# Kernel optimization log

Measured on AMD Instinct MI355X. Metric: run time of the kernel, lower is better.

The kernel has to match this reference:

```python
import jax, jax.numpy as jnp
import numpy as np

N, E, F_IN, D, D_OUT = 100000, 1600000, 64, 20, 16
EPS = 1e-5


def _mean_agg(x, src, dst, n):
    # gather source features, scatter-mean onto destination nodes
    s = jax.ops.segment_sum(x[src], dst, num_segments=n)
    cnt = jax.ops.segment_sum(jnp.ones((src.shape[0], 1), x.dtype), dst, num_segments=n)
    return s / jnp.maximum(cnt, 1.0)


def _batchnorm(h, g, b):
    mu = jnp.mean(h, axis=0)
    var = jnp.mean(jnp.square(h - mu), axis=0)  # biased variance, BatchNorm1d training math
    return (h - mu) * jax.lax.rsqrt(var + EPS) * g + b


def _block(x, src, dst, Wl, bl, Wr, Ws, bs, Wn, bn, g, be):
    # SAGEConv: lin_l(mean_agg) + lin_r(x); plus linskip; then lin, BN, ReLU
    agg = _mean_agg(x, src, dst, N)
    h = agg @ Wl + bl + x @ Wr + x @ Ws + bs
    h = h @ Wn + bn
    return jax.nn.relu(_batchnorm(h, g, be))


def setup_inputs() -> dict:
    key = jax.random.key(0)
    ks = jax.random.split(key, 32)
    sc = lambda fi: 1.0 / np.sqrt(fi)
    d = {}
    d["x"] = jax.random.normal(ks[0], (N, F_IN), jnp.float32)
    d["edge_index"] = jax.random.randint(ks[1], (2, E), 0, N, dtype=jnp.int64)
    d["edge_attr"] = jax.random.normal(ks[2], (E, 1), jnp.float32)
    # layer 1 (in = F_IN)
    d["Wl1"] = jax.random.normal(ks[3], (F_IN, D), jnp.float32) * sc(F_IN)
    d["bl1"] = jnp.zeros((D,), jnp.float32)
    d["Wr1"] = jax.random.normal(ks[4], (F_IN, D), jnp.float32) * sc(F_IN)
    d["Ws1"] = jax.random.normal(ks[5], (F_IN, D), jnp.float32) * sc(F_IN)
    d["bs1"] = jnp.zeros((D,), jnp.float32)
    d["Wn1"] = jax.random.normal(ks[6], (D, D), jnp.float32) * sc(D)
    d["bn1"] = jnp.zeros((D,), jnp.float32)
    d["g1"] = jnp.ones((D,), jnp.float32)
    d["be1"] = jnp.zeros((D,), jnp.float32)
    # layers 2-4 stacked (in = D)
    d["Wlm"] = jax.random.normal(ks[7], (3, D, D), jnp.float32) * sc(D)
    d["blm"] = jnp.zeros((3, D), jnp.float32)
    d["Wrm"] = jax.random.normal(ks[8], (3, D, D), jnp.float32) * sc(D)
    d["Wsm"] = jax.random.normal(ks[9], (3, D, D), jnp.float32) * sc(D)
    d["bsm"] = jnp.zeros((3, D), jnp.float32)
    d["Wnm"] = jax.random.normal(ks[10], (3, D, D), jnp.float32) * sc(D)
    d["bnm"] = jnp.zeros((3, D), jnp.float32)
    d["gm"] = jnp.ones((3, D), jnp.float32)
    d["bem"] = jnp.zeros((3, D), jnp.float32)
    # layer 5 (no BN/ReLU, out = D_OUT)
    d["Wl5"] = jax.random.normal(ks[11], (D, D), jnp.float32) * sc(D)
    d["bl5"] = jnp.zeros((D,), jnp.float32)
    d["Wr5"] = jax.random.normal(ks[12], (D, D), jnp.float32) * sc(D)
    d["Ws5"] = jax.random.normal(ks[13], (D, D), jnp.float32) * sc(D)
    d["bs5"] = jnp.zeros((D,), jnp.float32)
    d["Wn5"] = jax.random.normal(ks[14], (D, D_OUT), jnp.float32) * sc(D)
    d["bn5"] = jnp.zeros((D_OUT,), jnp.float32)
    return d


def reference(x, edge_index, edge_attr,
              Wl1, bl1, Wr1, Ws1, bs1, Wn1, bn1, g1, be1,
              Wlm, blm, Wrm, Wsm, bsm, Wnm, bnm, gm, bem,
              Wl5, bl5, Wr5, Ws5, bs5, Wn5, bn5):
    src, dst = edge_index[0], edge_index[1]
    # edge_attr is accepted by the torch forward but unused
    h = _block(x, src, dst, Wl1, bl1, Wr1, Ws1, bs1, Wn1, bn1, g1, be1)
    for i in range(3):  # layers 2-4
        h = _block(h, src, dst, Wlm[i], blm[i], Wrm[i], Wsm[i], bsm[i],
                   Wnm[i], bnm[i], gm[i], bem[i])
    # layer 5: sage + skip, final linear, no norm/relu
    agg = _mean_agg(h, src, dst, N)
    h = agg @ Wl5 + bl5 + h @ Wr5 + h @ Ws5 + bs5
    return h @ Wn5 + bn5
```

## Files before the change

### kernel.cpp

```cpp
#include <hip/hip_runtime.h>

constexpr int Nn   = 100000;
constexpr int Ne   = 1600000;
constexpr int FINN = 64;
constexpr int Dh   = 20;
constexpr int Dout = 16;
constexpr float EPSV = 1e-5f;

constexpr int NR  = 16;
constexpr int RSZ = Nn / NR;
constexpr int NSL = 32;
constexpr int P1B = 400;
constexpr int P1E = Ne / P1B;

constexpr size_t OFF_WC1  = 0;
constexpr size_t OFF_C1   = 2560;
constexpr size_t OFF_WCM  = 2592;
constexpr size_t OFF_CM   = 4992;
constexpr size_t OFF_WC5  = 5088;
constexpr size_t OFF_C5   = 5728;
constexpr size_t OFF_ST   = 5760;
constexpr size_t OFF_OFFS = 8192;
constexpr size_t OFF_BSUM = 208896;
constexpr size_t OFF_CNT  = 209408;
constexpr size_t OFF_CSR  = 309760;
constexpr size_t OFF_XA   = 1910784;
constexpr size_t OFF_XB   = 3510784;
constexpr size_t OFF_HP   = 5110784;
constexpr size_t OFF_BHT  = OFF_HP;
constexpr size_t OFF_OBHT = OFF_HP + 6400;
constexpr size_t OFF_RB   = OFF_HP + 12800;

__device__ inline unsigned short f2b(float x) {
    unsigned b = __float_as_uint(x);
    return (unsigned short)((b + 0x7FFFu + ((b >> 16) & 1u)) >> 16);
}
__device__ inline float b2f(unsigned short u) {
    return __uint_as_float(((unsigned)u) << 16);
}
__device__ inline float blo(unsigned u) { return __uint_as_float(u << 16); }
__device__ inline float bhi(unsigned u) { return __uint_as_float(u & 0xFFFF0000u); }
__device__ inline unsigned bpack(float lo, float hi) {
    return (unsigned)f2b(lo) | ((unsigned)f2b(hi) << 16);
}

__global__ void prep_weights(
    const float* __restrict__ Wl1, const float* __restrict__ bl1,
    const float* __restrict__ Wr1, const float* __restrict__ Ws1,
    const float* __restrict__ bs1, const float* __restrict__ Wn1,
    const float* __restrict__ bn1,
    const float* __restrict__ Wlm, const float* __restrict__ blm,
    const float* __restrict__ Wrm, const float* __restrict__ Wsm,
    const float* __restrict__ bsm, const float* __restrict__ Wnm,
    const float* __restrict__ bnm,
    const float* __restrict__ Wl5, const float* __restrict__ bl5,
    const float* __restrict__ Wr5, const float* __restrict__ Ws5,
    const float* __restrict__ bs5, const float* __restrict__ Wn5,
    const float* __restrict__ bn5,
    float* __restrict__ wc1, float* __restrict__ c1,
    float* __restrict__ wcm, float* __restrict__ cm,
    float* __restrict__ wc5, float* __restrict__ c5)
{
    int layer = blockIdx.x;
    int t = threadIdx.x;
    if (layer == 0) {
        for (int idx = t; idx < FINN * Dh; idx += blockDim.x) {
            int k = idx / Dh, j = idx % Dh;
            float a = 0.f, b = 0.f;
            for (int d = 0; d < Dh; ++d) {
                float wn = Wn1[d * Dh + j];
                a += Wl1[k * Dh + d] * wn;
                b += (Wr1[k * Dh + d] + Ws1[k * Dh + d]) * wn;
            }
            wc1[k * 40 + j] = a;
            wc1[k * 40 + 20 + j] = b;
        }
        for (int j = t; j < Dh; j += blockDim.x) {
            float c0 = 0.f;
            for (int d = 0; d < Dh; ++d) c0 += (bl1[d] + bs1[d]) * Wn1[d * Dh + j];
            c1[j] = c0 + bn1[j];
        }
    } else if (layer <= 3) {
        int i = layer - 1;
        const float* Wl = Wlm + i * Dh * Dh;
        const float* Wr = Wrm + i * Dh * Dh;
        const float* Ws = Wsm + i * Dh * Dh;
        const float* Wn = Wnm + i * Dh * Dh;
        const float* bl = blm + i * Dh;
        const float* bs = bsm + i * Dh;
        const float* bn = bnm + i * Dh;
        float* wc = wcm + i * 800;
        float* cc = cm + i * 32;
        for (int idx = t; idx < Dh * Dh; idx += blockDim.x) {
            int k = idx / Dh, j = idx % Dh;
            float a = 0.f, b = 0.f;
            for (int d = 0; d < Dh; ++d) {
                float wn = Wn[d * Dh + j];
                a += Wl[k * Dh + d] * wn;
                b += (Wr[k * Dh + d] + Ws[k * Dh + d]) * wn;
            }
            wc[k * 40 + j] = a;
            wc[k * 40 + 20 + j] = b;
        }
        for (int j = t; j < Dh; j += blockDim.x) {
            float c0 = 0.f;
            for (int d = 0; d < Dh; ++d) c0 += (bl[d] + bs[d]) * Wn[d * Dh + j];
            cc[j] = c0 + bn[j];
        }
    } else {
        for (int idx = t; idx < Dh * Dout; idx += blockDim.x) {
            int k = idx / Dout, j = idx % Dout;
            float a = 0.f, b = 0.f;
            for (int d = 0; d < Dh; ++d) {
                float wn = Wn5[d * Dout + j];
                a += Wl5[k * Dh + d] * wn;
                b += (Wr5[k * Dh + d] + Ws5[k * Dh + d]) * wn;
            }
            wc5[k * 32 + j] = a;
            wc5[k * 32 + 16 + j] = b;
        }
        for (int j = t; j < Dout; j += blockDim.x) {
            float c0 = 0.f;
            for (int d = 0; d < Dh; ++d) c0 += (bl5[d] + bs5[d]) * Wn5[d * Dout + j];
            c5[j] = c0 + bn5[j];
        }
    }
}

__global__ __launch_bounds__(256) void hist1(const int* __restrict__ dst, unsigned* __restrict__ bhT) {
    __shared__ unsigned h[16 * NR];
    int b = blockIdx.x, t = threadIdx.x;
    for (int i = t; i < 16 * NR; i += 256) h[i] = 0;
    __syncthreads();
    int sub = t & 15;
    int e0 = b * P1E, e1 = min(e0 + P1E, Ne);
    for (int e = e0 + t; e < e1; e += 256) {
        int r = dst[e] / RSZ;
        atomicAdd(&h[sub * NR + r], 1u);
    }
    __syncthreads();
    if (t < NR) {
        unsigned s = 0;
        for (int i = 0; i < 16; ++i) s += h[i * NR + t];
        bhT[t * P1B + b] = s;
    }
}

__global__ __launch_bounds__(1024) void scan1(
    const unsigned* __restrict__ bhT, unsigned* __restrict__ obhT, unsigned* __restrict__ rbase)
{
    __shared__ unsigned rtot[NR];
    int t = threadIdx.x;
    int w = t >> 6, lane = t & 63;
    constexpr int PER = (P1B + 63) / 64;
    if (w < NR) {
        unsigned v[PER];
        unsigned s = 0;
#pragma unroll
        for (int i = 0; i < PER; ++i) {
            int b = lane * PER + i;
            v[i] = (b < P1B) ? bhT[w * P1B + b] : 0u;
            s += v[i];
        }
        unsigned val = s;
        for (int off = 1; off < 64; off <<= 1) {
            unsigned u = __shfl_up(val, off, 64);
            if (lane >= off) val += u;
        }
        unsigned run = val - s;
#pragma unroll
        for (int i = 0; i < PER; ++i) {
            int b = lane * PER + i;
            if (b < P1B) obhT[w * P1B + b] = run;
            run += v[i];
        }
        if (lane == 63) rtot[w] = val;
    }
    __syncthreads();
    if (t == 0) {
        unsigned base = 0;
        for (int r = 0; r < NR; ++r) { rbase[r] = base; base += rtot[r]; }
        rbase[NR] = base;
    }
}

__global__ __launch_bounds__(256) void scatter1(
    const int* __restrict__ src, const int* __restrict__ dst,
    const unsigned* __restrict__ obhT, const unsigned* __restrict__ rbase,
    unsigned* __restrict__ ebuf)
{
    __shared__ unsigned cur[NR];
    int b = blockIdx.x, t = threadIdx.x;
    if (t < NR) cur[t] = rbase[t] + obhT[t * P1B + b];
    __syncthreads();
    int e0 = b * P1E, e1 = min(e0 + P1E, Ne);
    for (int e = e0 + t; e < e1; e += 256) {
        int d = dst[e];
        int r = d / RSZ;
        unsigned dl = (unsigned)(d - r * RSZ);
        unsigned pos = atomicAdd(&cur[r], 1u);
        ebuf[pos] = (dl << 17) | (unsigned)src[e];
    }
}

__global__ __launch_bounds__(256) void hist2(
    const unsigned* __restrict__ ebuf, const unsigned* __restrict__ rbase,
    unsigned short* __restrict__ part)
{
    __shared__ unsigned h[RSZ];
    int b = blockIdx.x, t = threadIdx.x;
    int r = b % NR, s = b / NR;
    for (int i = t; i < RSZ; i += 256) h[i] = 0;
    __syncthreads();
    unsigned lo = rbase[r], hi = rbase[r + 1];
    unsigned step = (hi - lo + NSL - 1) / NSL;
    unsigned e0 = lo + (unsigned)s * step;
    unsigned e1 = e0 + step; if (e1 > hi) e1 = hi;
    for (unsigned e = e0 + t; e < e1; e += 256)
        atomicAdd(&h[ebuf[e] >> 17], 1u);
    __syncthreads();
    unsigned short* p = part + (size_t)b * RSZ;
    for (int i = t; i < RSZ; i += 256) p[i] = (unsigned short)h[i];
}

__global__ void col_prefix(unsigned short* __restrict__ part, unsigned* __restrict__ cnt) {
    int d = blockIdx.x * blockDim.x + threadIdx.x;
    if (d >= Nn) return;
    int r = d / RSZ, dl = d - r * RSZ;
    unsigned run = 0;
#pragma unroll
    for (int s = 0; s < NSL; ++s) {
        size_t idx = ((size_t)s * NR + r) * RSZ + dl;
        unsigned v = part[idx];
        part[idx] = (unsigned short)run;
        run += v;
    }
    cnt[d] = run;
}

__global__ void scan_blocksums(const unsigned* __restrict__ cnt, unsigned* __restrict__ bsum, int n) {
    __shared__ unsigned sd[256];
    int b = blockIdx.x, t = threadIdx.x;
    int base = b * 1024;
    unsigned s = 0;
    for (int i = t; i < 1024; i += 256) {
        int idx = base + i;
        if (idx < n) s += cnt[idx];
    }
    sd[t] = s;
    __syncthreads();
    for (int off = 128; off > 0; off >>= 1) {
        if (t < off) sd[t] += sd[t + off];
        __syncthreads();
    }
    if (t == 0) bsum[b] = sd[0];
}

__global__ void scan_bsum(unsigned* __restrict__ bsum, int nb) {
    __shared__ unsigned sh[128];
    int t = threadIdx.x;
    unsigned v = (t < nb) ? bsum[t] : 0u;
    sh[t] = v;
    __syncthreads();
    for (int off = 1; off < 128; off <<= 1) {
        unsigned add = (t >= off) ? sh[t - off] : 0u;
        __syncthreads();
        sh[t] += add;
        __syncthreads();
    }
    if (t < nb) bsum[t] = sh[t] - v;
}

__global__ void scan_final(const unsigned* __restrict__ cnt, const unsigned* __restrict__ bsum,
                           unsigned* __restrict__ offs, int n) {
    __shared__ unsigned wsum[4], woff[4];
    int b = blockIdx.x, t = threadIdx.x;
    int base = b * 1024 + t * 4;
    unsigned v[4];
    unsigned s = 0;
#pragma unroll
    for (int i = 0; i < 4; ++i) {
        int idx = base + i;
        v[i] = (idx < n) ? cnt[idx] : 0u;
        s += v[i];
    }
    unsigned lane = t & 63;
    int w = t >> 6;
    unsigned val = s;
    for (int off = 1; off < 64; off <<= 1) {
        unsigned u = __shfl_up(val, off, 64);
        if (lane >= off) val += u;
    }
    if (lane == 63) wsum[w] = val;
    __syncthreads();
    if (t == 0) {
        unsigned r = 0;
        for (int i = 0; i < 4; ++i) { woff[i] = r; r += wsum[i]; }
    }
    __syncthreads();
    unsigned run = bsum[b] + woff[w] + (val - s);
#pragma unroll
    for (int i = 0; i < 4; ++i) {
        int idx = base + i;
        if (idx < n) {
            offs[idx] = run;
            run += v[i];
            if (idx == n - 1) offs[n] = run;
        }
    }
}

__global__ __launch_bounds__(256) void fill2(
    const unsigned* __restrict__ ebuf, const unsigned* __restrict__ rbase,
    const unsigned* __restrict__ offs, const unsigned short* __restrict__ part,
    unsigned* __restrict__ csr)
{
    __shared__ unsigned cur[RSZ];
    int b = blockIdx.x, t = threadIdx.x;
    int r = b % NR, s = b / NR;
    int lon = r * RSZ;
    const unsigned short* p = part + (size_t)b * RSZ;
    for (int i = t; i < RSZ; i += 256)
        cur[i] = offs[lon + i] + p[i];
    __syncthreads();
    unsigned lo = rbase[r], hi = rbase[r + 1];
    unsigned step = (hi - lo + NSL - 1) / NSL;
    unsigned e0 = lo + (unsigned)s * step;
    unsigned e1 = e0 + step; if (e1 > hi) e1 = hi;
    for (unsigned e = e0 + t; e < e1; e += 256) {
        unsigned v = ebuf[e];
        unsigned pos = atomicAdd(&cur[v >> 17], 1u);
        csr[pos] = v & 0x1FFFFu;
    }
}

template <int FINt, int FO, bool NORM, bool INBF16>
__global__ __launch_bounds__(256) void gemm_kernel(
    const void* __restrict__ xin_, const float* __restrict__ stats,
    const float* __restrict__ g, const float* __restrict__ be,
    const float* __restrict__ wc, const float* __restrict__ cvec,
    unsigned short* __restrict__ xa, unsigned short* __restrict__ xb)
{
    constexpr int XS  = ((FO + 7) / 8) * 8;
    constexpr int XSI = ((FINt + 7) / 8) * 8;
    constexpr int CH  = XS / 8;
    constexpr int CL  = 2 * CH;
    __shared__ float swl[FINt * 2 * FO + 8];
    __shared__ float sscale[Dh], sshift[Dh];
    int t = threadIdx.x;
    for (int i = t; i < FINt * 2 * FO; i += 256) swl[i] = wc[i];
    if (t < 8) swl[FINt * 2 * FO + t] = 0.f;
    if (NORM) {
        if (t < Dh) {
            float mu = stats[t] * (1.0f / Nn);
            float var = stats[32 + t] * (1.0f / Nn) - mu * mu;
            float sc = g[t] * rsqrtf(var + EPSV);
            sscale[t] = sc;
            sshift[t] = be[t] - mu * sc;
        }
    }
    __syncthreads();
    int tid = blockIdx.x * 256 + t;
    int n = tid / CL;
    int c = tid % CL;
    if (n >= Nn) return;
    int half = c / CH, cc = c % CH;
    int off = half * FO + cc * 8;
    int jmax = (cc == CH - 1) ? (FO - (CH - 1) * 8) : 8;

    float acc[8];
#pragma unroll
    for (int j = 0; j < 8; ++j) acc[j] = 0.f;

#pragma unroll
    for (int k4 = 0; k4 < FINt / 4; ++k4) {
        float xs[4];
        if (INBF16) {
            const unsigned short* xr = (const unsigned short*)xin_ + (size_t)n * XSI;
            ushort4 v = *(const ushort4*)(xr + 4 * k4);
            xs[0] = b2f(v.x); xs[1] = b2f(v.y); xs[2] = b2f(v.z); xs[3] = b2f(v.w);
        } else {
            const float* xr = (const float*)xin_ + (size_t)n * FINt;
            float4 v = *(const float4*)(xr + 4 * k4);
            xs[0] = v.x; xs[1] = v.y; xs[2] = v.z; xs[3] = v.w;
        }
        if (NORM) {
#pragma unroll
            for (int kk = 0; kk < 4; ++kk)
                xs[kk] = fmaxf(xs[kk] * sscale[4 * k4 + kk] + sshift[4 * k4 + kk], 0.0f);
        }
#pragma unroll
        for (int kk = 0; kk < 4; ++kk) {
            float xk = xs[kk];
            const float* wr = &swl[(4 * k4 + kk) * (2 * FO) + off];
#pragma unroll
            for (int j = 0; j < 8; ++j) acc[j] = fmaf(xk, wr[j], acc[j]);
        }
    }

    float hv[8];
#pragma unroll
    for (int j = 0; j < 8; ++j) hv[j] = acc[j];
    if (half) {
#pragma unroll
        for (int j = 0; j < 8; ++j) hv[j] += cvec[cc * 8 + j];
    }
#pragma unroll
    for (int j = 0; j < 8; ++j) if (j >= jmax) hv[j] = 0.f;

    unsigned short* dstp = (half ? xb : xa) + (size_t)n * XS + cc * 8;
    uint4 w;
    w.x = bpack(hv[0], hv[1]); w.y = bpack(hv[2], hv[3]);
    w.z = bpack(hv[4], hv[5]); w.w = bpack(hv[6], hv[7]);
    *(uint4*)dstp = w;
}

template <int F, bool WITH_STATS, bool OUTBF16>
__global__ __launch_bounds__(256) void pull_kernel(
    const unsigned* __restrict__ offs, const unsigned* __restrict__ csr,
    const unsigned short* __restrict__ xa, const unsigned short* __restrict__ xb,
    void* __restrict__ out_, float* __restrict__ stats)
{
    constexpr int C  = (F + 7) / 8;
    constexpr int XS = C * 8;
    __shared__ float sstat[2 * F];
    int t = threadIdx.x;
    if (WITH_STATS) {
        if (t < 2 * F) sstat[t] = 0.f;
        __syncthreads();
    }
    int tid = blockIdx.x * blockDim.x + t;
    int n = tid / C;
    int c = tid % C;
    int valid = (c == C - 1) ? (F - 8 * (C - 1)) : 8;
    bool act = (n < Nn);
    float h[8];
    if (act) {
        unsigned b = offs[n], e = offs[n + 1];
        const unsigned short* base = xa + c * 8;
        float acc[8];
#pragma unroll
        for (int j = 0; j < 8; ++j) acc[j] = 0.f;
        for (unsigned k = b; k < e; k += 16) {
            unsigned s[16];
            float m[16];
#pragma unroll
            for (int i = 0; i < 16; ++i) {
                unsigned kk = k + i;
                bool in = kk < e;
                s[i] = csr[in ? kk : b];
                m[i] = in ? 1.0f : 0.0f;
            }
            uint4 v[16];
#pragma unroll
            for (int i = 0; i < 16; ++i) v[i] = *(const uint4*)(base + (size_t)s[i] * XS);
#pragma unroll
            for (int i = 0; i < 16; ++i) {
                acc[0] = fmaf(m[i], blo(v[i].x), acc[0]);
                acc[1] = fmaf(m[i], bhi(v[i].x), acc[1]);
                acc[2] = fmaf(m[i], blo(v[i].y), acc[2]);
                acc[3] = fmaf(m[i], bhi(v[i].y), acc[3]);
                acc[4] = fmaf(m[i], blo(v[i].z), acc[4]);
                acc[5] = fmaf(m[i], bhi(v[i].z), acc[5]);
                acc[6] = fmaf(m[i], blo(v[i].w), acc[6]);
                acc[7] = fmaf(m[i], bhi(v[i].w), acc[7]);
            }
        }
        float inv = 1.0f / fmaxf((float)(e - b), 1.0f);
        uint4 xv = *(const uint4*)(xb + (size_t)n * XS + c * 8);
        float xf[8] = { blo(xv.x), bhi(xv.x), blo(xv.y), bhi(xv.y),
                        blo(xv.z), bhi(xv.z), blo(xv.w), bhi(xv.w) };
#pragma unroll
        for (int j = 0; j < 8; ++j) h[j] = fmaf(acc[j], inv, xf[j]);
        if (OUTBF16) {
            unsigned short* o = (unsigned short*)out_ + (size_t)n * XS + c * 8;
            if (valid == 8) {
                uint4 w;
                w.x = bpack(h[0], h[1]); w.y = bpack(h[2], h[3]);
                w.z = bpack(h[4], h[5]); w.w = bpack(h[6], h[7]);
                *(uint4*)o = w;
            } else {
                ushort4 w4;
                w4.x = f2b(h[0]); w4.y = f2b(h[1]); w4.z = f2b(h[2]); w4.w = f2b(h[3]);
                *(ushort4*)o = w4;
            }
        } else {
            float* o = (float*)out_ + (size_t)n * F + c * 8;
            float4 v0; v0.x = h[0]; v0.y = h[1]; v0.z = h[2]; v0.w = h[3];
            *(float4*)o = v0;
            if (valid == 8) {
                float4 v1; v1.x = h[4]; v1.y = h[5]; v1.z = h[6]; v1.w = h[7];
                *(float4*)(o + 4) = v1;
            }
        }
    }
    if (WITH_STATS) {
        if (act) {
            for (int j = 0; j < valid; ++j) {
                atomicAdd(&sstat[c * 8 + j], h[j]);
                atomicAdd(&sstat[F + c * 8 + j], h[j] * h[j]);
            }
        }
        __syncthreads();
        if (t < F) {
            atomicAdd(&stats[t], sstat[t]);
        } else if (t < 2 * F) {
            atomicAdd(&stats[32 + (t - F)], sstat[t]);
        }
    }
}

extern "C" void kernel_launch(void* const* d_in, const int* in_sizes, int n_in,
                              void* d_out, int out_size, void* d_ws, size_t ws_size,
                              hipStream_t stream) {
    const float* x   = (const float*)d_in[0];
    const int* ei    = (const int*)d_in[1];
    const int* esrc  = ei;
    const int* edst  = ei + Ne;
    const float* Wl1 = (const float*)d_in[3];
    const float* bl1 = (const float*)d_in[4];
    const float* Wr1 = (const float*)d_in[5];
    const float* Ws1 = (const float*)d_in[6];
    const float* bs1 = (const float*)d_in[7];
    const float* Wn1 = (const float*)d_in[8];
    const float* bn1 = (const float*)d_in[9];
    const float* g1  = (const float*)d_in[10];
    const float* be1 = (const float*)d_in[11];
    const float* Wlm = (const float*)d_in[12];
    const float* blm = (const float*)d_in[13];
    const float* Wrm = (const float*)d_in[14];
    const float* Wsm = (const float*)d_in[15];
    const float* bsm = (const float*)d_in[16];
    const float* Wnm = (const float*)d_in[17];
    const float* bnm = (const float*)d_in[18];
    const float* gm  = (const float*)d_in[19];
    const float* bem = (const float*)d_in[20];
    const float* Wl5 = (const float*)d_in[21];
    const float* bl5 = (const float*)d_in[22];
    const float* Wr5 = (const float*)d_in[23];
    const float* Ws5 = (const float*)d_in[24];
    const float* bs5 = (const float*)d_in[25];
    const float* Wn5 = (const float*)d_in[26];
    const float* bn5 = (const float*)d_in[27];

    float* ws   = (float*)d_ws;
    unsigned* u = (unsigned*)d_ws;
    float* wc1   = ws + OFF_WC1;
    float* c1    = ws + OFF_C1;
    float* wcm   = ws + OFF_WCM;
    float* cm    = ws + OFF_CM;
    float* wc5   = ws + OFF_WC5;
    float* c5    = ws + OFF_C5;
    float* stats = ws + OFF_ST;
    unsigned* offs = u + OFF_OFFS;
    unsigned* bsum = u + OFF_BSUM;
    unsigned* cnt  = u + OFF_CNT;
    unsigned* csr  = u + OFF_CSR;
    unsigned short* xa = (unsigned short*)(ws + OFF_XA);
    unsigned* ebuf = u + OFF_XA;
    unsigned short* xb = (unsigned short*)(ws + OFF_XB);
    unsigned short* part = (unsigned short*)(ws + OFF_XB);
    unsigned short* hp = (unsigned short*)(ws + OFF_HP);
    unsigned* bhT  = u + OFF_BHT;
    unsigned* obhT = u + OFF_OBHT;
    unsigned* rbase = u + OFF_RB;

    hipMemsetAsync(stats, 0, 256 * sizeof(float), stream);

    prep_weights<<<5, 256, 0, stream>>>(Wl1, bl1, Wr1, Ws1, bs1, Wn1, bn1,
                                        Wlm, blm, Wrm, Wsm, bsm, Wnm, bnm,
                                        Wl5, bl5, Wr5, Ws5, bs5, Wn5, bn5,
                                        wc1, c1, wcm, cm, wc5, c5);

    hist1<<<P1B, 256, 0, stream>>>(edst, bhT);
    scan1<<<1, 1024, 0, stream>>>(bhT, obhT, rbase);
    scatter1<<<P1B, 256, 0, stream>>>(esrc, edst, obhT, rbase, ebuf);
    hist2<<<NR * NSL, 256, 0, stream>>>(ebuf, rbase, part);
    col_prefix<<<(Nn + 255) / 256, 256, 0, stream>>>(part, cnt);
    constexpr int NB = (Nn + 1023) / 1024;
    scan_blocksums<<<NB, 256, 0, stream>>>(cnt, bsum, Nn);
    scan_bsum<<<1, 128, 0, stream>>>(bsum, NB);
    scan_final<<<NB, 256, 0, stream>>>(cnt, bsum, offs, Nn);
    fill2<<<NR * NSL, 256, 0, stream>>>(ebuf, rbase, offs, part, csr);

    int gblk20 = (Nn * 6 + 255) / 256;
    int gblk16 = (Nn * 4 + 255) / 256;
    int pblk20 = (Nn * 3 + 255) / 256;
    int pblk16 = (Nn * 2 + 255) / 256;

    gemm_kernel<FINN, Dh, false, false><<<gblk20, 256, 0, stream>>>(x, nullptr, nullptr, nullptr, wc1, c1, xa, xb);
    pull_kernel<Dh, true, true><<<pblk20, 256, 0, stream>>>(offs, csr, xa, xb, hp, stats + 0);
    gemm_kernel<Dh, Dh, true, true><<<gblk20, 256, 0, stream>>>(hp, stats + 0, g1, be1, wcm + 0, cm + 0, xa, xb);
    pull_kernel<Dh, true, true><<<pblk20, 256, 0, stream>>>(offs, csr, xa, xb, hp, stats + 64);
    gemm_kernel<Dh, Dh, true, true><<<gblk20, 256, 0, stream>>>(hp, stats + 64, gm + 0, bem + 0, wcm + 800, cm + 32, xa, xb);
    pull_kernel<Dh, true, true><<<pblk20, 256, 0, stream>>>(offs, csr, xa, xb, hp, stats + 128);
    gemm_kernel<Dh, Dh, true, true><<<gblk20, 256, 0, stream>>>(hp, stats + 128, gm + 20, bem + 20, wcm + 1600, cm + 64, xa, xb);
    pull_kernel<Dh, true, true><<<pblk20, 256, 0, stream>>>(offs, csr, xa, xb, hp, stats + 192);
    gemm_kernel<Dh, Dout, true, true><<<gblk16, 256, 0, stream>>>(hp, stats + 192, gm + 40, bem + 40, wc5, c5, xa, xb);
    pull_kernel<Dout, false, false><<<pblk16, 256, 0, stream>>>(offs, csr, xa, xb, d_out, nullptr);
}
```

Before: 344.5 us.

## Split each node's edge list across two thread groups and reduce via shuffle

The pull aggregation kernel now gives each node 8 threads: two halves of its edge range, with up to 4 feature chunks each. The partial sums are combined with a cross-lane shuffle. The unroll depth drops from 16 to 8 gathers per iteration. This is meant to cut per-thread serial latency on high-degree nodes and expose more parallelism, at the cost of idle lanes when C<4 (F=20 uses 3 of 4 chunk slots, F=16 uses 2) and more threads launched.

```diff
diff --git a/kernel.cpp b/kernel.cpp
--- a/kernel.cpp
+++ b/kernel.cpp
@@ -423,39 +423,48 @@
 {
     constexpr int C  = (F + 7) / 8;
     constexpr int XS = C * 8;
+    constexpr int TPN = 8;
     __shared__ float sstat[2 * F];
     int t = threadIdx.x;
     if (WITH_STATS) {
         if (t < 2 * F) sstat[t] = 0.f;
         __syncthreads();
     }
-    int tid = blockIdx.x * blockDim.x + t;
-    int n = tid / C;
-    int c = tid % C;
+    int tid = blockIdx.x * 256 + t;
+    int n = tid / TPN;
+    int sub = tid % TPN;
+    int s = sub >> 2;
+    int c = sub & 3;
+    bool cact = (c < C);
+    bool act = (n < Nn);
     int valid = (c == C - 1) ? (F - 8 * (C - 1)) : 8;
-    bool act = (n < Nn);
-    float h[8];
-    if (act) {
-        unsigned b = offs[n], e = offs[n + 1];
+
+    float acc[8];
+#pragma unroll
+    for (int j = 0; j < 8; ++j) acc[j] = 0.f;
+    unsigned b = 0, e = 0;
+    if (act) { b = offs[n]; e = offs[n + 1]; }
+    if (act && cact && e > b) {
+        unsigned len = e - b;
+        unsigned hl = (len + 1) >> 1;
+        unsigned k0 = b + (s ? hl : 0u);
+        unsigned k1 = s ? e : (b + hl);
         const unsigned short* base = xa + c * 8;
-        float acc[8];
-#pragma unroll
-        for (int j = 0; j < 8; ++j) acc[j] = 0.f;
-        for (unsigned k = b; k < e; k += 16) {
-            unsigned s[16];
-            float m[16];
-#pragma unroll
-            for (int i = 0; i < 16; ++i) {
+        for (unsigned k = k0; k < k1; k += 8) {
+            unsigned si[8];
+            float m[8];
+#pragma unroll
+            for (int i = 0; i < 8; ++i) {
                 unsigned kk = k + i;
-                bool in = kk < e;
-                s[i] = csr[in ? kk : b];
+                bool in = kk < k1;
+                si[i] = csr[in ? kk : b];
                 m[i] = in ? 1.0f : 0.0f;
             }
-            uint4 v[16];
-#pragma unroll
-            for (int i = 0; i < 16; ++i) v[i] = *(const uint4*)(base + (size_t)s[i] * XS);
-#pragma unroll
-            for (int i = 0; i < 16; ++i) {
+            uint4 v[8];
+#pragma unroll
+            for (int i = 0; i < 8; ++i) v[i] = *(const uint4*)(base + (size_t)si[i] * XS);
+#pragma unroll
+            for (int i = 0; i < 8; ++i) {
                 acc[0] = fmaf(m[i], blo(v[i].x), acc[0]);
                 acc[1] = fmaf(m[i], bhi(v[i].x), acc[1]);
                 acc[2] = fmaf(m[i], blo(v[i].y), acc[2]);
@@ -466,6 +475,12 @@
                 acc[7] = fmaf(m[i], bhi(v[i].w), acc[7]);
             }
         }
+    }
+#pragma unroll
+    for (int j = 0; j < 8; ++j) acc[j] += __shfl_xor(acc[j], 4, 64);
+
+    float h[8];
+    if (act && cact && s == 0) {
         float inv = 1.0f / fmaxf((float)(e - b), 1.0f);
         uint4 xv = *(const uint4*)(xb + (size_t)n * XS + c * 8);
         float xf[8] = { blo(xv.x), bhi(xv.x), blo(xv.y), bhi(xv.y),
@@ -495,7 +510,7 @@
         }
     }
     if (WITH_STATS) {
-        if (act) {
+        if (act && cact && s == 0) {
             for (int j = 0; j < valid; ++j) {
                 atomicAdd(&sstat[c * 8 + j], h[j]);
                 atomicAdd(&sstat[F + c * 8 + j], h[j] * h[j]);
@@ -585,17 +600,16 @@
 
     int gblk20 = (Nn * 6 + 255) / 256;
     int gblk16 = (Nn * 4 + 255) / 256;
-    int pblk20 = (Nn * 3 + 255) / 256;
-    int pblk16 = (Nn * 2 + 255) / 256;
+    int pblk   = (Nn * 8 + 255) / 256;
 
     gemm_kernel<FINN, Dh, false, false><<<gblk20, 256, 0, stream>>>(x, nullptr, nullptr, nullptr, wc1, c1, xa, xb);
-    pull_kernel<Dh, true, true><<<pblk20, 256, 0, stream>>>(offs, csr, xa, xb, hp, stats + 0);
+    pull_kernel<Dh, true, true><<<pblk, 256, 0, stream>>>(offs, csr, xa, xb, hp, stats + 0);
     gemm_kernel<Dh, Dh, true, true><<<gblk20, 256, 0, stream>>>(hp, stats + 0, g1, be1, wcm + 0, cm + 0, xa, xb);
-    pull_kernel<Dh, true, true><<<pblk20, 256, 0, stream>>>(offs, csr, xa, xb, hp, stats + 64);
+    pull_kernel<Dh, true, true><<<pblk, 256, 0, stream>>>(offs, csr, xa, xb, hp, stats + 64);
     gemm_kernel<Dh, Dh, true, true><<<gblk20, 256, 0, stream>>>(hp, stats + 64, gm + 0, bem + 0, wcm + 800, cm + 32, xa, xb);
-    pull_kernel<Dh, true, true><<<pblk20, 256, 0, stream>>>(offs, csr, xa, xb, hp, stats + 128);
+    pull_kernel<Dh, true, true><<<pblk, 256, 0, stream>>>(offs, csr, xa, xb, hp, stats + 128);
     gemm_kernel<Dh, Dh, true, true><<<gblk20, 256, 0, stream>>>(hp, stats + 128, gm + 20, bem + 20, wcm + 1600, cm + 64, xa, xb);
-    pull_kernel<Dh, true, true><<<pblk20, 256, 0, stream>>>(offs, csr, xa, xb, hp, stats + 192);
+    pull_kernel<Dh, true, true><<<pblk, 256, 0, stream>>>(offs, csr, xa, xb, hp, stats + 192);
     gemm_kernel<Dh, Dout, true, true><<<gblk16, 256, 0, stream>>>(hp, stats + 192, gm + 40, bem + 40, wc5, c5, xa, xb);
-    pull_kernel<Dout, false, false><<<pblk16, 256, 0, stream>>>(offs, csr, xa, xb, d_out, nullptr);
-}
+    pull_kernel<Dout, false, false><<<pblk, 256, 0, stream>>>(offs, csr, xa, xb, d_out, nullptr);
+}
```

Measured after the change: 491.9 us. +42.8%, slower.
